# Optimization experiments

Hardware: AMD Instinct MI355X
Metric: run time of the kernel (lower is better)

Reference implementation:

```python
import jax, jax.numpy as jnp
import numpy as np
from jax import lax


def _transform_points(pts, M, eps=1e-8):
    # pytorch3d row-vector convention: p' = [p, 1] @ M, then perspective divide by w.
    ph = jnp.concatenate([pts, jnp.ones(pts.shape[:-1] + (1,), pts.dtype)], axis=-1)
    out = jnp.einsum('bnk,bkl->bnl', ph, M)
    w = out[..., 3:4]
    w = jnp.where(jnp.abs(w) < eps, eps, w)
    return out[..., :3] / w


def _rasterize_spheres(pts_screen, radius, image_size, K):
    # pts_screen: [B,N,3] with (x,y) in NDC and z = view-space depth; radius: [B,N].
    # Per pixel: keep K front-most (smallest z>0) points with NDC dist2 <= radius^2.
    B, N, _ = pts_screen.shape
    half = 1.0 - 1.0 / image_size
    coords = jnp.linspace(half, -half, image_size, dtype=pts_screen.dtype)  # pytorch3d NDC: +x left, +y up
    py, px = jnp.meshgrid(coords, coords, indexing='ij')  # [H,W]
    dx = pts_screen[:, None, None, :, 0] - px[None, :, :, None]  # [B,H,W,N]
    dy = pts_screen[:, None, None, :, 1] - py[None, :, :, None]
    dist2 = dx * dx + dy * dy
    z = pts_screen[:, None, None, :, 2]  # [B,1,1,N]
    inside = (dist2 <= (radius * radius)[:, None, None, :]) & (z > 0)
    zmask = jnp.where(inside, z, jnp.inf)
    negz, inds = lax.top_k(-zmask, K)  # K smallest z (front-most) per pixel
    valid = jnp.isfinite(negz)
    zbuf = jnp.where(valid, -negz, jnp.float32(-1.0))
    d2 = jnp.take_along_axis(dist2, inds, axis=-1)
    dists = jnp.where(valid, d2, jnp.float32(-1.0))
    idx = jnp.where(valid, inds, -1)
    return idx, zbuf, dists


def setup_inputs() -> dict:
    key = jax.random.key(0)
    k1, k2 = jax.random.split(key)
    B, N = 1, 1024
    points = jax.random.normal(k1, (B, N, 3), dtype=jnp.float32)
    radius = 0.02 + 0.06 * jax.random.uniform(k2, (B, N), dtype=jnp.float32)
    # Rigid world->view: identity rotation, translate camera so points sit at z ~ 3 (row-vector convention).
    w2v = np.eye(4, dtype=np.float32)
    w2v[3, 2] = 3.0
    world2view = jnp.asarray(w2v)[None]
    # Perspective projection (row-vector): [x,y,z,1] @ P = [s x, s y, a z + b, z]
    s, znear, zfar = 2.0, 0.1, 100.0
    a = zfar / (zfar - znear)
    b = -zfar * znear / (zfar - znear)
    proj = jnp.asarray(np.array([[s, 0, 0, 0], [0, s, 0, 0], [0, 0, a, 1], [0, 0, b, 0]], dtype=np.float32))[None]
    return {'points': points, 'radius': radius, 'world2view': world2view, 'proj': proj,
            'image_size': 256, 'points_per_pixel': 8}


def reference(points, radius, world2view, proj, image_size, points_per_pixel):
    pts_view = _transform_points(points, world2view)
    pts_screen = _transform_points(pts_view, proj)
    pts_screen = pts_screen.at[..., 2].set(pts_view[..., 2])  # keep view-space depth
    idx, zbuf, dists = _rasterize_spheres(pts_screen, radius, image_size, points_per_pixel)
    return idx, zbuf, dists
```

## Files before the change

kernel.cpp:

```cpp
#include <hip/hip_runtime.h>
#include <math.h>


#define KPP 8
#define TS  16

__global__ __launch_bounds__(256) void sphere_raster_kernel(
    const float* __restrict__ points,
    const float* __restrict__ radius,
    const float* __restrict__ w2v,
    const float* __restrict__ proj,
    float* __restrict__ out,
    int B, int N, int H, int W)
{
    extern __shared__ char smem[];
    float4* sh   = (float4*)smem;
    float4* cmp  = (float4*)(smem + (size_t)N * 16);
    int*    cidx = (int*)(smem + (size_t)N * 16 + (size_t)(N + 8) * 16);
    __shared__ int wsum[4];

    const int tid      = threadIdx.x;
    const int tilesX   = W / TS;
    const int tilesPer = tilesX * (H / TS);
    const int tile     = blockIdx.x % tilesPer;
    const int b        = blockIdx.x / tilesPer;
    const int tx0      = (tile % tilesX) * TS;
    const int ty0      = (tile / tilesX) * TS;
    const int j        = tx0 + (tid & (TS - 1));
    const int i        = ty0 + (tid >> 4);
    const int lane     = tid & 63;
    const int wid      = tid >> 6;

    const float* M1 = w2v  + (size_t)b * 16;
    const float* M2 = proj + (size_t)b * 16;

    const double halfd = 1.0 - 1.0 / (double)W;
    const double stepd = 2.0 * halfd / (double)(W - 1);
    const float px = (float)(halfd - (double)j * stepd);
    const float py = (float)(halfd - (double)i * stepd);
    const float cx = (float)(halfd - ((double)tx0 + (TS - 1) * 0.5) * stepd);
    const float cy = (float)(halfd - ((double)ty0 + (TS - 1) * 0.5) * stepd);
    const float hext = (float)(((TS - 1) * 0.5 + 1.0) * stepd);

    const int t0 = tid * 4;
    int mask = 0, c = 0;
#pragma unroll 1
    for (int s = 0; s < 4; ++s) {
        const int t = t0 + s;
        const float* pp = points + ((size_t)b * N + t) * 3;
        float x = pp[0], y = pp[1], z = pp[2];
        float vx = ((x * M1[0] + y * M1[4]) + z * M1[8])  + M1[12];
        float vy = ((x * M1[1] + y * M1[5]) + z * M1[9])  + M1[13];
        float vz = ((x * M1[2] + y * M1[6]) + z * M1[10]) + M1[14];
        float vw = ((x * M1[3] + y * M1[7]) + z * M1[11]) + M1[15];
        float w1 = (fabsf(vw) < 1e-8f) ? 1e-8f : vw;
        vx /= w1; vy /= w1; vz /= w1;
        float sx = ((vx * M2[0] + vy * M2[4]) + vz * M2[8])  + M2[12];
        float sy = ((vx * M2[1] + vy * M2[5]) + vz * M2[9])  + M2[13];
        float sw = ((vx * M2[3] + vy * M2[7]) + vz * M2[11]) + M2[15];
        float w2 = (fabsf(sw) < 1e-8f) ? 1e-8f : sw;
        sx /= w2; sy /= w2;
        float r = radius[(size_t)b * N + t];
        float r2eff = (vz > 0.0f) ? r * r : -1.0f;
        sh[t] = make_float4(sx, sy, vz, r2eff);
        float dxm = fmaxf(0.0f, fabsf(sx - cx) - hext);
        float dym = fmaxf(0.0f, fabsf(sy - cy) - hext);
        float dmin2 = dxm * dxm + dym * dym;
        int keep = (dmin2 <= r2eff + 1e-6f) ? 1 : 0;
        mask |= keep << s;
        c += keep;
    }

    int pre = c;
#pragma unroll
    for (int d = 1; d < 64; d <<= 1) {
        int v = __shfl_up(pre, d);
        if (lane >= d) pre += v;
    }
    if (lane == 63) wsum[wid] = pre;
    __syncthreads();
    int wbase = 0, M = 0;
#pragma unroll
    for (int w = 0; w < 4; ++w) {
        int s = wsum[w];
        if (w < wid) wbase += s;
        M += s;
    }
    int pos = wbase + (pre - c);
#pragma unroll 1
    for (int s = 0; s < 4; ++s) {
        if ((mask >> s) & 1) { cmp[pos] = sh[t0 + s]; cidx[pos] = t0 + s; ++pos; }
    }
    const int Mpad = (M + 3) & ~3;
    if (tid < Mpad - M) {
        cmp[M + tid]  = make_float4(0.0f, 0.0f, 0.0f, -1.0f);
        cidx[M + tid] = -1;
    }
    __syncthreads();

    float zb[KPP]; int id[KPP]; float dd[KPP];
#pragma unroll
    for (int k = 0; k < KPP; ++k) { zb[k] = INFINITY; id[k] = -1; dd[k] = -1.0f; }

    auto test1 = [&](float4 p, int ic0) {
        float dx = p.x - px;
        float dy = p.y - py;
        float dist2 = __fadd_rn(__fmul_rn(dx, dx), __fmul_rn(dy, dy));
        if ((dist2 <= p.w) && (p.z < zb[KPP - 1])) {
            float zc = p.z; int ic = ic0; float dc = dist2;
#pragma unroll
            for (int k2 = 0; k2 < KPP; ++k2) {
                bool lt = (zc < zb[k2]);
                float tz = zb[k2]; int ti = id[k2]; float td = dd[k2];
                if (lt) { zb[k2] = zc; id[k2] = ic; dd[k2] = dc; zc = tz; ic = ti; dc = td; }
            }
        }
    };

#pragma unroll 1
    for (int n = 0; n < Mpad; n += 4) {
        float4 p0 = cmp[n], p1 = cmp[n + 1], p2 = cmp[n + 2], p3 = cmp[n + 3];
        int4 i4 = *(const int4*)&cidx[n];
        test1(p0, i4.x);
        test1(p1, i4.y);
        test1(p2, i4.z);
        test1(p3, i4.w);
    }

    const size_t pix   = ((size_t)b * H + i) * W + j;
    const size_t plane = (size_t)B * H * W * KPP;
    float vidx[KPP], vzbf[KPP], vdst[KPP];
#pragma unroll
    for (int k = 0; k < KPP; ++k) {
        bool valid = (zb[k] != INFINITY);
        vidx[k] = valid ? (float)id[k] : -1.0f;
        vzbf[k] = valid ? zb[k]        : -1.0f;
        vdst[k] = valid ? dd[k]        : -1.0f;
    }
    float* oidx = out + pix * KPP;
    float* ozbf = out + plane + pix * KPP;
    float* odst = out + 2 * plane + pix * KPP;
    *(float4*)(oidx)     = make_float4(vidx[0], vidx[1], vidx[2], vidx[3]);
    *(float4*)(oidx + 4) = make_float4(vidx[4], vidx[5], vidx[6], vidx[7]);
    *(float4*)(ozbf)     = make_float4(vzbf[0], vzbf[1], vzbf[2], vzbf[3]);
    *(float4*)(ozbf + 4) = make_float4(vzbf[4], vzbf[5], vzbf[6], vzbf[7]);
    *(float4*)(odst)     = make_float4(vdst[0], vdst[1], vdst[2], vdst[3]);
    *(float4*)(odst + 4) = make_float4(vdst[4], vdst[5], vdst[6], vdst[7]);
}

extern "C" void kernel_launch(void* const* d_in, const int* in_sizes, int n_in,
                              void* d_out, int out_size, void* d_ws, size_t ws_size,
                              hipStream_t stream) {
    const float* points = (const float*)d_in[0];
    const float* radius = (const float*)d_in[1];
    const float* w2v    = (const float*)d_in[2];
    const float* proj   = (const float*)d_in[3];
    int B = in_sizes[2] / 16;
    if (B < 1) B = 1;
    int N = in_sizes[1] / B;
    int HW = out_size / (3 * B * KPP);
    int H = 1;
    while ((H + 1) * (H + 1) <= HW) ++H;
    int W = H;

    int tiles = (W / TS) * (H / TS);
    size_t shmem = (size_t)N * 16 + (size_t)(N + 8) * 16 + (size_t)(N + 8) * 4;
    sphere_raster_kernel<<<B * tiles, 256, shmem, stream>>>(
        points, radius, w2v, proj, (float*)d_out, B, N, H, W);
}
```

Measured before the change: 15.25 us.

## Pre-sort tile candidates by depth with a wave bitonic sort and early-exit scan

When a tile has at most 64 candidate points, one wavefront bitonic-sorts them by depth (ties broken by index) into shared memory. Each pixel then walks the sorted list, takes the first K hits in order, and stops once every lane has K. This replaces the per-hit insertion sort. Point and radius loads are also vectorised into float4, and the staging copy of all transformed points is removed, which shrinks shared memory. The risks are the added sort and barrier, scalar output stores in the fast path, and a fallback to the old loop for dense tiles.

```diff
diff --git a/kernel.cpp b/kernel.cpp
--- a/kernel.cpp
+++ b/kernel.cpp
@@ -14,9 +14,10 @@
     int B, int N, int H, int W)
 {
     extern __shared__ char smem[];
-    float4* sh   = (float4*)smem;
-    float4* cmp  = (float4*)(smem + (size_t)N * 16);
-    int*    cidx = (int*)(smem + (size_t)N * 16 + (size_t)(N + 8) * 16);
+    float4* cmp  = (float4*)smem;
+    int*    cidx = (int*)(smem + (size_t)(N + 64) * 16);
+    float4* srt  = (float4*)(smem + (size_t)(N + 64) * 20);
+    int*    sidx = (int*)(smem + (size_t)(N + 64) * 20 + 1024);
     __shared__ int wsum[4];
 
     const int tid      = threadIdx.x;
@@ -43,12 +44,21 @@
     const float hext = (float)(((TS - 1) * 0.5 + 1.0) * stepd);
 
     const int t0 = tid * 4;
-    int mask = 0, c = 0;
-#pragma unroll 1
+    float4 P[4];
+    int keep[4];
+    int c = 0;
+
+    const float4* pv = (const float4*)(points + ((size_t)b * N + t0) * 3);
+    float4 q0 = pv[0], q1 = pv[1], q2 = pv[2];
+    float4 rr = *(const float4*)(radius + (size_t)b * N + t0);
+    float xs[4] = {q0.x, q0.w, q1.z, q2.y};
+    float ys[4] = {q0.y, q1.x, q1.w, q2.z};
+    float zs[4] = {q0.z, q1.y, q2.x, q2.w};
+    float rv[4] = {rr.x, rr.y, rr.z, rr.w};
+
+#pragma unroll
     for (int s = 0; s < 4; ++s) {
-        const int t = t0 + s;
-        const float* pp = points + ((size_t)b * N + t) * 3;
-        float x = pp[0], y = pp[1], z = pp[2];
+        float x = xs[s], y = ys[s], z = zs[s];
         float vx = ((x * M1[0] + y * M1[4]) + z * M1[8])  + M1[12];
         float vy = ((x * M1[1] + y * M1[5]) + z * M1[9])  + M1[13];
         float vz = ((x * M1[2] + y * M1[6]) + z * M1[10]) + M1[14];
@@ -60,15 +70,14 @@
         float sw = ((vx * M2[3] + vy * M2[7]) + vz * M2[11]) + M2[15];
         float w2 = (fabsf(sw) < 1e-8f) ? 1e-8f : sw;
         sx /= w2; sy /= w2;
-        float r = radius[(size_t)b * N + t];
+        float r = rv[s];
         float r2eff = (vz > 0.0f) ? r * r : -1.0f;
-        sh[t] = make_float4(sx, sy, vz, r2eff);
         float dxm = fmaxf(0.0f, fabsf(sx - cx) - hext);
         float dym = fmaxf(0.0f, fabsf(sy - cy) - hext);
         float dmin2 = dxm * dxm + dym * dym;
-        int keep = (dmin2 <= r2eff + 1e-6f) ? 1 : 0;
-        mask |= keep << s;
-        c += keep;
+        keep[s] = (dmin2 <= r2eff + 1e-6f) ? 1 : 0;
+        P[s] = make_float4(sx, sy, vz, r2eff);
+        c += keep[s];
     }
 
     int pre = c;
@@ -87,16 +96,76 @@
         M += s;
     }
     int pos = wbase + (pre - c);
-#pragma unroll 1
+#pragma unroll
     for (int s = 0; s < 4; ++s) {
-        if ((mask >> s) & 1) { cmp[pos] = sh[t0 + s]; cidx[pos] = t0 + s; ++pos; }
-    }
-    const int Mpad = (M + 3) & ~3;
-    if (tid < Mpad - M) {
-        cmp[M + tid]  = make_float4(0.0f, 0.0f, 0.0f, -1.0f);
-        cidx[M + tid] = -1;
+        if (keep[s]) { cmp[pos] = P[s]; cidx[pos] = t0 + s; ++pos; }
+    }
+    const int padTo = (M <= 64) ? 64 : ((M + 3) & ~3);
+    if (tid < padTo - M) {
+        cmp[M + tid]  = make_float4(0.0f, 0.0f, INFINITY, -1.0f);
+        cidx[M + tid] = 0x7fffffff;
     }
     __syncthreads();
+
+    const size_t pix   = ((size_t)b * H + i) * W + j;
+    const size_t plane = (size_t)B * H * W * KPP;
+    float* oidx = out + pix * KPP;
+    float* ozbf = out + plane + pix * KPP;
+    float* odst = out + 2 * plane + pix * KPP;
+
+    if (M <= 64) {
+        if (wid == 0) {
+            float z  = cmp[lane].z;
+            int   k2 = cidx[lane];
+            int   sl = lane;
+#pragma unroll
+            for (int k = 2; k <= 64; k <<= 1) {
+#pragma unroll
+                for (int jj = k >> 1; jj > 0; jj >>= 1) {
+                    float oz  = __shfl_xor(z, jj);
+                    int   ok2 = __shfl_xor(k2, jj);
+                    int   osl = __shfl_xor(sl, jj);
+                    bool keepMin = ((lane & jj) == 0) == ((lane & k) == 0);
+                    bool lt = (z < oz) || (z == oz && k2 < ok2);
+                    bool mine = keepMin ? lt : !lt;
+                    z  = mine ? z  : oz;
+                    k2 = mine ? k2 : ok2;
+                    sl = mine ? sl : osl;
+                }
+            }
+            srt[lane]  = cmp[sl];
+            sidx[lane] = cidx[sl];
+        }
+        __syncthreads();
+
+        int cnt = 0;
+        for (int n = 0; n < M; n += 8) {
+            float4 pr[8];
+#pragma unroll
+            for (int u = 0; u < 8; ++u) pr[u] = srt[n + u];
+            int4 a4 = *(const int4*)&sidx[n];
+            int4 b4 = *(const int4*)&sidx[n + 4];
+            int ir[8] = {a4.x, a4.y, a4.z, a4.w, b4.x, b4.y, b4.z, b4.w};
+#pragma unroll
+            for (int u = 0; u < 8; ++u) {
+                float dx = pr[u].x - px;
+                float dy = pr[u].y - py;
+                float dist2 = __fadd_rn(__fmul_rn(dx, dx), __fmul_rn(dy, dy));
+                if ((dist2 <= pr[u].w) && (cnt < KPP)) {
+                    oidx[cnt] = (float)ir[u];
+                    ozbf[cnt] = pr[u].z;
+                    odst[cnt] = dist2;
+                    ++cnt;
+                }
+            }
+            if (__all(cnt >= KPP)) break;
+        }
+#pragma unroll
+        for (int k = 0; k < KPP; ++k) {
+            if (k >= cnt) { oidx[k] = -1.0f; ozbf[k] = -1.0f; odst[k] = -1.0f; }
+        }
+        return;
+    }
 
     float zb[KPP]; int id[KPP]; float dd[KPP];
 #pragma unroll
@@ -118,7 +187,7 @@
     };
 
 #pragma unroll 1
-    for (int n = 0; n < Mpad; n += 4) {
+    for (int n = 0; n < padTo; n += 4) {
         float4 p0 = cmp[n], p1 = cmp[n + 1], p2 = cmp[n + 2], p3 = cmp[n + 3];
         int4 i4 = *(const int4*)&cidx[n];
         test1(p0, i4.x);
@@ -127,8 +196,6 @@
         test1(p3, i4.w);
     }
 
-    const size_t pix   = ((size_t)b * H + i) * W + j;
-    const size_t plane = (size_t)B * H * W * KPP;
     float vidx[KPP], vzbf[KPP], vdst[KPP];
 #pragma unroll
     for (int k = 0; k < KPP; ++k) {
@@ -137,9 +204,6 @@
         vzbf[k] = valid ? zb[k]        : -1.0f;
         vdst[k] = valid ? dd[k]        : -1.0f;
     }
-    float* oidx = out + pix * KPP;
-    float* ozbf = out + plane + pix * KPP;
-    float* odst = out + 2 * plane + pix * KPP;
     *(float4*)(oidx)     = make_float4(vidx[0], vidx[1], vidx[2], vidx[3]);
     *(float4*)(oidx + 4) = make_float4(vidx[4], vidx[5], vidx[6], vidx[7]);
     *(float4*)(ozbf)     = make_float4(vzbf[0], vzbf[1], vzbf[2], vzbf[3]);
@@ -164,7 +228,7 @@
     int W = H;
 
     int tiles = (W / TS) * (H / TS);
-    size_t shmem = (size_t)N * 16 + (size_t)(N + 8) * 16 + (size_t)(N + 8) * 4;
+    size_t shmem = (size_t)(N + 64) * 20 + 64 * 20;
     sphere_raster_kernel<<<B * tiles, 256, shmem, stream>>>(
         points, radius, w2v, proj, (float*)d_out, B, N, H, W);
 }
```

New measurement: 14.75 us. 3.3% less time.
